# Optimization experiments

Hardware: AMD Instinct MI355X
Metric: run time of the kernel (lower is better)

Reference implementation:

```python
import jax, jax.numpy as jnp
import numpy as np

B, N, D, H, DH = 2, 2048, 1024, 16, 64
INNER = H * DH          # 1024
FF_INNER = 4 * D        # 4096 (GEGLU)
EPS = 1e-5


def setup_inputs() -> dict:
    key = jax.random.key(0)
    ks = jax.random.split(key, 12)
    s = D ** -0.5
    return {
        "x": jax.random.normal(ks[0], (B, N, D), jnp.float32),
        "Wq": jax.random.normal(ks[1], (D, INNER), jnp.float32) * s,
        "Wk": jax.random.normal(ks[2], (D, INNER), jnp.float32) * s,
        "Wv": jax.random.normal(ks[3], (D, INNER), jnp.float32) * s,
        "Wo": jax.random.normal(ks[4], (INNER, D), jnp.float32) * s,
        "bo": jnp.zeros((D,), jnp.float32),
        "ln1_g": jnp.ones((D,), jnp.float32),
        "ln1_b": jnp.zeros((D,), jnp.float32),
        "ln3_g": jnp.ones((D,), jnp.float32),
        "ln3_b": jnp.zeros((D,), jnp.float32),
        "Wff1": jax.random.normal(ks[5], (D, 2 * FF_INNER), jnp.float32) * s,
        "bff1": jnp.zeros((2 * FF_INNER,), jnp.float32),
        "Wff2": jax.random.normal(ks[6], (FF_INNER, D), jnp.float32) * (FF_INNER ** -0.5),
        "bff2": jnp.zeros((D,), jnp.float32),
    }


def _layernorm(x, g, b):
    mu = jnp.mean(x, axis=-1, keepdims=True)
    var = jnp.mean(jnp.square(x - mu), axis=-1, keepdims=True)
    return (x - mu) * jax.lax.rsqrt(var + EPS) * g + b


def reference(x, Wq, Wk, Wv, Wo, bo, ln1_g, ln1_b, ln3_g, ln3_b, Wff1, bff1, Wff2, bff2):
    scale = DH ** -0.5

    # norm1 + self-attention (attn1)
    x_features = _layernorm(x, ln1_g, ln1_b)
    q = (x_features @ Wq).reshape(B, N, H, DH)
    k = (x_features @ Wk).reshape(B, N, H, DH)
    v = (x_features @ Wv).reshape(B, N, H, DH)
    sim = jnp.einsum('bihd,bjhd->bhij', q, k) * scale      # (B,H,N,N) full scores
    attn = jax.nn.softmax(sim, axis=-1)
    inter_out = jnp.einsum('bhij,bjhd->bhid', attn, v)     # (B,H,N,DH)
    out = inter_out.transpose(0, 2, 1, 3).reshape(B, N, INNER)
    attended_x = out @ Wo + bo
    x = attended_x + x

    # norm3 + GEGLU feed-forward
    h = _layernorm(x, ln3_g, ln3_b) @ Wff1 + bff1
    a, gate = h[..., :FF_INNER], h[..., FF_INNER:]
    x = (a * jax.nn.gelu(gate, approximate=False)) @ Wff2 + bff2 + x

    # match torch return: q,k,v as (b h) n d, attn = inter_out (b h n d)
    q_bh = q.transpose(0, 2, 1, 3).reshape(B * H, N, DH)
    k_bh = k.transpose(0, 2, 1, 3).reshape(B * H, N, DH)
    v_bh = v.transpose(0, 2, 1, 3).reshape(B * H, N, DH)
    return (x, q_bh, k_bh, v_bh, inter_out, x_features)
```

## Files before the change

### kernel.cpp

```cpp
#include <hip/hip_runtime.h>
#include <hip/hip_bf16.h>

#define B_ 2
#define N_ 2048
#define D_ 1024
#define H_ 16
#define DH_ 64
#define M_ 4096
#define FFI_ 4096

typedef __attribute__((ext_vector_type(8))) short bh8;
typedef __attribute__((ext_vector_type(4))) float f4;

#define DEV static __device__ __forceinline__

DEV short f2bf(float f) { __hip_bfloat16 h = __float2bfloat16(f); return *reinterpret_cast<short*>(&h); }
DEV float bf2f(short s) { __hip_bfloat16 h = *reinterpret_cast<__hip_bfloat16*>(&s); return __bfloat162float(h); }

#define GLDS(gp, lp) __builtin_amdgcn_global_load_lds((const __attribute__((address_space(1))) void*)(gp), (__attribute__((address_space(3))) void*)(lp), 16, 0, 0)
#define MFMA16(a,b,c) __builtin_amdgcn_mfma_f32_16x16x32_bf16(a,b,c,0,0,0)

__global__ __launch_bounds__(256) void ln_kernel(const float* __restrict__ x,
    const float* __restrict__ g, const float* __restrict__ b,
    float* __restrict__ outF, short* __restrict__ outB)
{
  const int row = blockIdx.x;
  const int t = threadIdx.x;
  const float4 v = reinterpret_cast<const float4*>(x + (long)row*D_)[t];
  float s = v.x+v.y+v.z+v.w;
  float sq = v.x*v.x+v.y*v.y+v.z*v.z+v.w*v.w;
  #pragma unroll
  for (int o=32;o>0;o>>=1){ s += __shfl_xor(s,o); sq += __shfl_xor(sq,o); }
  __shared__ float red[8];
  const int w = t>>6, l = t&63;
  if (l==0){ red[w]=s; red[4+w]=sq; }
  __syncthreads();
  s  = red[0]+red[1]+red[2]+red[3];
  sq = red[4]+red[5]+red[6]+red[7];
  const float mu = s*(1.f/D_);
  const float rstd = rsqrtf(sq*(1.f/D_) - mu*mu + 1e-5f);
  const float4 gv = reinterpret_cast<const float4*>(g)[t];
  const float4 bv = reinterpret_cast<const float4*>(b)[t];
  float4 y;
  y.x=(v.x-mu)*rstd*gv.x+bv.x; y.y=(v.y-mu)*rstd*gv.y+bv.y;
  y.z=(v.z-mu)*rstd*gv.z+bv.z; y.w=(v.w-mu)*rstd*gv.w+bv.w;
  if (outF) reinterpret_cast<float4*>(outF + (long)row*D_)[t] = y;
  short4 ys; ys.x=f2bf(y.x); ys.y=f2bf(y.y); ys.z=f2bf(y.z); ys.w=f2bf(y.w);
  reinterpret_cast<short4*>(outB + (long)row*D_)[t] = ys;
}

__global__ __launch_bounds__(256) void transpose_cast(const float* __restrict__ in,
    short* __restrict__ out, int R, int C)
{
  __shared__ float tile[32][33];
  const int tx = threadIdx.x & 31, ty = threadIdx.x >> 5;
  const int c0 = blockIdx.x*32, r0 = blockIdx.y*32;
  #pragma unroll
  for (int i=0;i<4;i++) tile[ty+i*8][tx] = in[(long)(r0+ty+i*8)*C + c0+tx];
  __syncthreads();
  #pragma unroll
  for (int i=0;i<4;i++) out[(long)(c0+ty+i*8)*R + r0+tx] = f2bf(tile[tx][ty+i*8]);
}

DEV void gemm_core(const short* __restrict__ A, const short* __restrict__ BT, int K,
                   int m0, int n0, short* lA, short* lB, f4 (&acc)[4][4])
{
  const int t = threadIdx.x, w = t>>6, l = t&63;
  const int wrow = (w>>1)*64, wcol = (w&1)*64;
  const int lr = l&15, lk = (l>>4)*8;
  const int sr = t>>2, sc = (t&3)*8;
  const short* gA = A  + (long)(m0+sr)*K + sc;
  const short* gB = BT + (long)(n0+sr)*K + sc;
  #pragma unroll
  for (int i=0;i<4;i++)
    #pragma unroll
    for (int j=0;j<4;j++) acc[i][j] = f4{0.f,0.f,0.f,0.f};
  for (int k0=0; k0<K; k0+=32) {
    __syncthreads();
    GLDS(gA,              &lA[w*512]);
    GLDS(gA + (long)64*K, &lA[2048 + w*512]);
    GLDS(gB,              &lB[w*512]);
    GLDS(gB + (long)64*K, &lB[2048 + w*512]);
    gA += 32; gB += 32;
    asm volatile("s_waitcnt vmcnt(0)" ::: "memory");
    __syncthreads();
    bh8 af[4], bf_[4];
    #pragma unroll
    for (int i=0;i<4;i++) af[i]  = *reinterpret_cast<const bh8*>(&lA[(wrow+i*16+lr)*32 + lk]);
    #pragma unroll
    for (int j=0;j<4;j++) bf_[j] = *reinterpret_cast<const bh8*>(&lB[(wcol+j*16+lr)*32 + lk]);
    #pragma unroll
    for (int i=0;i<4;i++)
      #pragma unroll
      for (int j=0;j<4;j++)
        acc[i][j] = MFMA16(af[i], bf_[j], acc[i][j]);
  }
}

__global__ __launch_bounds__(256) void gemm_qkv(const short* __restrict__ A,
    const short* __restrict__ BTq, const short* __restrict__ BTk, const short* __restrict__ BTv,
    float* __restrict__ oQ, float* __restrict__ oK, float* __restrict__ oV,
    short* __restrict__ bQ, short* __restrict__ bK, short* __restrict__ bV)
{
  __shared__ short lA[4096], lB[4096];
  const int m0 = blockIdx.x*128;
  const int by = blockIdx.y, sel = by>>3, n0 = (by&7)*128;
  const short* BT = sel==0 ? BTq : (sel==1 ? BTk : BTv);
  float* oF = sel==0 ? oQ : (sel==1 ? oK : oV);
  short* oB = sel==0 ? bQ : (sel==1 ? bK : bV);
  const float bscale = sel==0 ? 0.125f : 1.0f;
  f4 acc[4][4];
  gemm_core(A, BT, 1024, m0, n0, lA, lB, acc);
  const int t = threadIdx.x, w = t>>6, l = t&63;
  const int wrow=(w>>1)*64, wcol=(w&1)*64, lr=l&15;
  #pragma unroll
  for (int i=0;i<4;i++)
    #pragma unroll
    for (int j=0;j<4;j++)
      #pragma unroll
      for (int r=0;r<4;r++) {
        const int grow = m0 + wrow + i*16 + (l>>4)*4 + r;
        const int gcol = n0 + wcol + j*16 + lr;
        const int bb = grow >> 11, nn = grow & 2047;
        const int hh = gcol >> 6, dd = gcol & 63;
        const long oi = ((long)(bb*H_ + hh)*N_ + nn)*DH_ + dd;
        const float v = acc[i][j][r];
        oF[oi] = v;
        oB[oi] = f2bf(v * bscale);
      }
}

template<int MODE>
__global__ __launch_bounds__(256) void gemm_bt(const short* __restrict__ A,
    const short* __restrict__ BT, int Ndim, int K,
    const float* __restrict__ bias, const float* __restrict__ resid,
    float* __restrict__ outF, short* __restrict__ outB)
{
  __shared__ short lA[4096], lB[4096];
  const int m0 = blockIdx.x*128, n0 = blockIdx.y*128;
  f4 acc[4][4];
  gemm_core(A, BT, K, m0, n0, lA, lB, acc);
  const int t = threadIdx.x, w=t>>6, l=t&63;
  const int wrow=(w>>1)*64, wcol=(w&1)*64, lr=l&15;
  #pragma unroll
  for (int i=0;i<4;i++)
    #pragma unroll
    for (int j=0;j<4;j++)
      #pragma unroll
      for (int r=0;r<4;r++) {
        const int grow = m0 + wrow + i*16 + (l>>4)*4 + r;
        const int gcol = n0 + wcol + j*16 + lr;
        const long oi = (long)grow*Ndim + gcol;
        const float v = acc[i][j][r] + bias[gcol];
        if (MODE==1) outF[oi] = v + resid[oi];
        else         outB[oi] = f2bf(v);
      }
}

__global__ __launch_bounds__(256) void attn_kernel(const short* __restrict__ Q,
    const short* __restrict__ Kb, const short* __restrict__ Vb,
    float* __restrict__ interOut, short* __restrict__ attnB)
{
  __shared__ short Kt[64*72];
  __shared__ short Vt[64*72];
  __shared__ short Pt[4*16*72];
  const int t = threadIdx.x, w = t>>6, l = t&63;
  const int bh = blockIdx.y;
  const int q0 = blockIdx.x*64;
  const int lr = l&15, lk = (l>>4)*8;
  const long base = (long)bh * (N_*DH_);
  const int qrow = q0 + w*16;
  bh8 qf0 = *reinterpret_cast<const bh8*>(&Q[base + (long)(qrow+lr)*DH_ + lk]);
  bh8 qf1 = *reinterpret_cast<const bh8*>(&Q[base + (long)(qrow+lr)*DH_ + 32 + lk]);
  f4 o[4];
  #pragma unroll
  for (int i=0;i<4;i++) o[i]=f4{0.f,0.f,0.f,0.f};
  float m_run[4], l_run[4];
  #pragma unroll
  for (int r=0;r<4;r++){ m_run[r]=-1e30f; l_run[r]=0.f; }
  const int srow = t>>3, sd = (t&7)*8;
  short* Pw = &Pt[w*16*72];
  for (int kt=0; kt<N_/64; kt++) {
    __syncthreads();
    #pragma unroll
    for (int it=0; it<2; it++) {
      const int j = it*32 + srow;
      const long grow = base + (long)(kt*64 + j)*DH_ + sd;
      int4 kv = *reinterpret_cast<const int4*>(&Kb[grow]);
      *reinterpret_cast<int4*>(&Kt[j*72 + sd]) = kv;
      int4 vv = *reinterpret_cast<const int4*>(&Vb[grow]);
      const short* vs = reinterpret_cast<const short*>(&vv);
      #pragma unroll
      for (int e=0;e<8;e++) Vt[(sd+e)*72 + j] = vs[e];
    }
    __syncthreads();
    f4 s[4];
    #pragma unroll
    for (int cb=0;cb<4;cb++) {
      bh8 kf0 = *reinterpret_cast<const bh8*>(&Kt[(cb*16+lr)*72 + lk]);
      bh8 kf1 = *reinterpret_cast<const bh8*>(&Kt[(cb*16+lr)*72 + 32 + lk]);
      f4 z = f4{0.f,0.f,0.f,0.f};
      z = MFMA16(qf0, kf0, z);
      z = MFMA16(qf1, kf1, z);
      s[cb] = z;
    }
    float mx[4];
    #pragma unroll
    for (int r=0;r<4;r++) mx[r] = fmaxf(fmaxf(s[0][r],s[1][r]), fmaxf(s[2][r],s[3][r]));
    #pragma unroll
    for (int mk=1; mk<16; mk<<=1)
      #pragma unroll
      for (int r=0;r<4;r++) mx[r] = fmaxf(mx[r], __shfl_xor(mx[r], mk));
    float rs[4];
    #pragma unroll
    for (int r=0;r<4;r++) {
      const float mn = fmaxf(m_run[r], mx[r]);
      const float al = __expf(m_run[r]-mn);
      m_run[r] = mn;
      l_run[r] *= al;
      float sum = 0.f;
      #pragma unroll
      for (int cb=0;cb<4;cb++) {
        const float pv = __expf(s[cb][r]-mn);
        sum += pv;
        Pw[((l>>4)*4 + r)*72 + cb*16 + lr] = f2bf(pv);
      }
      rs[r] = sum;
      #pragma unroll
      for (int cb=0;cb<4;cb++) o[cb][r] *= al;
    }
    #pragma unroll
    for (int mk=1; mk<16; mk<<=1)
      #pragma unroll
      for (int r=0;r<4;r++) rs[r] += __shfl_xor(rs[r], mk);
    #pragma unroll
    for (int r=0;r<4;r++) l_run[r] += rs[r];
    asm volatile("s_waitcnt lgkmcnt(0)" ::: "memory");
    __builtin_amdgcn_sched_barrier(0);
    bh8 pa0 = *reinterpret_cast<const bh8*>(&Pw[lr*72 + lk]);
    bh8 pa1 = *reinterpret_cast<const bh8*>(&Pw[lr*72 + 32 + lk]);
    #pragma unroll
    for (int db=0; db<4; db++) {
      bh8 vf0 = *reinterpret_cast<const bh8*>(&Vt[(db*16+lr)*72 + lk]);
      bh8 vf1 = *reinterpret_cast<const bh8*>(&Vt[(db*16+lr)*72 + 32 + lk]);
      o[db] = MFMA16(pa0, vf0, o[db]);
      o[db] = MFMA16(pa1, vf1, o[db]);
    }
  }
  const int bb = bh>>4, hh = bh&15;
  #pragma unroll
  for (int db=0; db<4; db++)
    #pragma unroll
    for (int r=0;r<4;r++) {
      const int n = qrow + (l>>4)*4 + r;
      const int d = db*16 + lr;
      const float v = o[db][r] / l_run[r];
      interOut[base + (long)n*DH_ + d] = v;
      attnB[((long)(bb*N_ + n))*D_*0 + ((long)(bb*N_ + n))*1024 + hh*DH_ + d] = f2bf(v);
    }
}

__global__ __launch_bounds__(256) void gelu_mul(const short* __restrict__ h, short* __restrict__ g)
{
  const long i = ((long)blockIdx.x*256 + threadIdx.x)*8;
  const long m = i >> 12;
  const int j = (int)(i & 4095);
  bh8 av = *reinterpret_cast<const bh8*>(&h[m*8192 + j]);
  bh8 gv = *reinterpret_cast<const bh8*>(&h[m*8192 + 4096 + j]);
  bh8 ov;
  #pragma unroll
  for (int e=0;e<8;e++) {
    const float a  = bf2f(av[e]);
    const float xg = bf2f(gv[e]);
    const float ge = 0.5f*xg*(1.f + erff(xg*0.70710678118f));
    ov[e] = f2bf(a*ge);
  }
  *reinterpret_cast<bh8*>(&g[i]) = ov;
}

extern "C" void kernel_launch(void* const* d_in, const int* in_sizes, int n_in,
                              void* d_out, int out_size, void* d_ws, size_t ws_size,
                              hipStream_t stream)
{
  const float* x    = (const float*)d_in[0];
  const float* Wq   = (const float*)d_in[1];
  const float* Wk   = (const float*)d_in[2];
  const float* Wv   = (const float*)d_in[3];
  const float* Wo   = (const float*)d_in[4];
  const float* bo   = (const float*)d_in[5];
  const float* ln1g = (const float*)d_in[6];
  const float* ln1b = (const float*)d_in[7];
  const float* ln3g = (const float*)d_in[8];
  const float* ln3b = (const float*)d_in[9];
  const float* Wff1 = (const float*)d_in[10];
  const float* bff1 = (const float*)d_in[11];
  const float* Wff2 = (const float*)d_in[12];
  const float* bff2 = (const float*)d_in[13];
  float* out = (float*)d_out;
  const long SZ = (long)M_*D_;
  float* out_x     = out;
  float* out_q     = out + SZ;
  float* out_k     = out + 2*SZ;
  float* out_v     = out + 3*SZ;
  float* out_inter = out + 4*SZ;
  float* out_xf    = out + 5*SZ;

  char* p = (char*)d_ws;
  auto alloc = [&](size_t bytes){ void* r = (void*)p; p += (bytes + 255) & ~(size_t)255; return r; };
  short* xf_bf  = (short*)alloc(SZ*2);
  short* q_bf   = (short*)alloc(SZ*2);
  short* k_bf   = (short*)alloc(SZ*2);
  short* v_bf   = (short*)alloc(SZ*2);
  short* at_bf  = (short*)alloc(SZ*2);
  float* x2     = (float*)alloc(SZ*4);
  short* x2n_bf = (short*)alloc(SZ*2);
  short* h_bf   = (short*)alloc((size_t)M_*8192*2);
  short* g_bf   = (short*)alloc((size_t)M_*4096*2);
  short* WqT    = (short*)alloc((size_t)1024*1024*2);
  short* WkT    = (short*)alloc((size_t)1024*1024*2);
  short* WvT    = (short*)alloc((size_t)1024*1024*2);
  short* WoT    = (short*)alloc((size_t)1024*1024*2);
  short* Wff1T  = (short*)alloc((size_t)8192*1024*2);
  short* Wff2T  = (short*)alloc((size_t)1024*4096*2);
  (void)in_sizes; (void)n_in; (void)out_size; (void)ws_size;

  dim3 blk(256);
  transpose_cast<<<dim3(32,32),  blk, 0, stream>>>(Wq,   WqT,   1024, 1024);
  transpose_cast<<<dim3(32,32),  blk, 0, stream>>>(Wk,   WkT,   1024, 1024);
  transpose_cast<<<dim3(32,32),  blk, 0, stream>>>(Wv,   WvT,   1024, 1024);
  transpose_cast<<<dim3(32,32),  blk, 0, stream>>>(Wo,   WoT,   1024, 1024);
  transpose_cast<<<dim3(256,32), blk, 0, stream>>>(Wff1, Wff1T, 1024, 8192);
  transpose_cast<<<dim3(32,128), blk, 0, stream>>>(Wff2, Wff2T, 4096, 1024);
  ln_kernel<<<M_, blk, 0, stream>>>(x, ln1g, ln1b, out_xf, xf_bf);
  gemm_qkv<<<dim3(32,24), blk, 0, stream>>>(xf_bf, WqT, WkT, WvT,
                                            out_q, out_k, out_v, q_bf, k_bf, v_bf);
  attn_kernel<<<dim3(32,32), blk, 0, stream>>>(q_bf, k_bf, v_bf, out_inter, at_bf);
  gemm_bt<1><<<dim3(32,8),  blk, 0, stream>>>(at_bf,  WoT,   1024, 1024, bo,   x,   x2,    nullptr);
  ln_kernel<<<M_, blk, 0, stream>>>(x2, ln3g, ln3b, nullptr, x2n_bf);
  gemm_bt<2><<<dim3(32,64), blk, 0, stream>>>(x2n_bf, Wff1T, 8192, 1024, bff1, nullptr, nullptr, h_bf);
  gelu_mul<<<8192, blk, 0, stream>>>(h_bf, g_bf);
  gemm_bt<1><<<dim3(32,8),  blk, 0, stream>>>(g_bf,   Wff2T, 1024, 4096, bff2, x2,  out_x, nullptr);
}
```

Measured before the change: 656.6 us.

## Swizzle attention K/V LDS tiles and load K via global_load_lds

Replaces the padded K and V shared-memory tiles with XOR-swizzled unpadded layouts. K is now loaded directly into LDS with global_load_lds, and V uses a swizzled transpose store. MFMA sections are wrapped in s_setprio raises. The goal is to cut LDS bank conflicts and register staging for K, at the cost of more complex index math and an explicit vmcnt wait.

```diff
diff --git a/kernel.cpp b/kernel.cpp
--- a/kernel.cpp
+++ b/kernel.cpp
@@ -161,13 +161,13 @@
     const short* __restrict__ Kb, const short* __restrict__ Vb,
     float* __restrict__ interOut, short* __restrict__ attnB)
 {
-  __shared__ short Kt[64*72];
-  __shared__ short Vt[64*72];
+  __shared__ short Kt[64*64];
+  __shared__ short Vt[64*64];
   __shared__ short Pt[4*16*72];
   const int t = threadIdx.x, w = t>>6, l = t&63;
   const int bh = blockIdx.y;
   const int q0 = blockIdx.x*64;
-  const int lr = l&15, lk = (l>>4)*8;
+  const int lr = l&15, lk = (l>>4)*8, g = l>>4;
   const long base = (long)bh * (N_*DH_);
   const int qrow = q0 + w*16;
   bh8 qf0 = *reinterpret_cast<const bh8*>(&Q[base + (long)(qrow+lr)*DH_ + lk]);
@@ -178,32 +178,48 @@
   float m_run[4], l_run[4];
   #pragma unroll
   for (int r=0;r<4;r++){ m_run[r]=-1e30f; l_run[r]=0.f; }
-  const int srow = t>>3, sd = (t&7)*8;
   short* Pw = &Pt[w*16*72];
+  const char* ldsK = (const char*)Kt;
+  const int beta0 = w*2048 + l*16;
+  const int srow = t>>3, sdp = t&7, sd = sdp*8;
   for (int kt=0; kt<N_/64; kt++) {
     __syncthreads();
+    {
+      const char* Kg = (const char*)(Kb + base + (long)kt*64*DH_);
+      #pragma unroll
+      for (int i=0;i<2;i++) {
+        const int beta = beta0 + i*1024;
+        const int krow = beta>>7, kpch = (beta>>4)&7;
+        GLDS(Kg + krow*128 + (kpch ^ (krow&7))*16, (char*)Kt + (w*2+i)*1024);
+      }
+    }
     #pragma unroll
     for (int it=0; it<2; it++) {
       const int j = it*32 + srow;
-      const long grow = base + (long)(kt*64 + j)*DH_ + sd;
-      int4 kv = *reinterpret_cast<const int4*>(&Kb[grow]);
-      *reinterpret_cast<int4*>(&Kt[j*72 + sd]) = kv;
-      int4 vv = *reinterpret_cast<const int4*>(&Vb[grow]);
+      const int4 vv = *reinterpret_cast<const int4*>(&Vb[base + (long)(kt*64+j)*DH_ + sd]);
       const short* vs = reinterpret_cast<const short*>(&vv);
-      #pragma unroll
-      for (int e=0;e<8;e++) Vt[(sd+e)*72 + j] = vs[e];
-    }
+      const int cb0 = (it*4 + (srow>>3)) ^ sdp;
+      const int jc  = srow & 7;
+      #pragma unroll
+      for (int e=0;e<8;e++)
+        Vt[(sd+e)*64 + ((cb0^e)<<3) + jc] = vs[e];
+    }
+    asm volatile("s_waitcnt vmcnt(0)" ::: "memory");
     __syncthreads();
     f4 s[4];
+    __builtin_amdgcn_s_setprio(1);
     #pragma unroll
     for (int cb=0;cb<4;cb++) {
-      bh8 kf0 = *reinterpret_cast<const bh8*>(&Kt[(cb*16+lr)*72 + lk]);
-      bh8 kf1 = *reinterpret_cast<const bh8*>(&Kt[(cb*16+lr)*72 + 32 + lk]);
+      const int krow = cb*16+lr;
+      const char* kr = ldsK + krow*128;
+      bh8 kf0 = *reinterpret_cast<const bh8*>(kr + ((g  )^(lr&7))*16);
+      bh8 kf1 = *reinterpret_cast<const bh8*>(kr + ((g+4)^(lr&7))*16);
       f4 z = f4{0.f,0.f,0.f,0.f};
       z = MFMA16(qf0, kf0, z);
       z = MFMA16(qf1, kf1, z);
       s[cb] = z;
     }
+    __builtin_amdgcn_s_setprio(0);
     float mx[4];
     #pragma unroll
     for (int r=0;r<4;r++) mx[r] = fmaxf(fmaxf(s[0][r],s[1][r]), fmaxf(s[2][r],s[3][r]));
@@ -240,11 +256,17 @@
     bh8 pa0 = *reinterpret_cast<const bh8*>(&Pw[lr*72 + lk]);
     bh8 pa1 = *reinterpret_cast<const bh8*>(&Pw[lr*72 + 32 + lk]);
     #pragma unroll
-    for (int db=0; db<4; db++) {
-      bh8 vf0 = *reinterpret_cast<const bh8*>(&Vt[(db*16+lr)*72 + lk]);
-      bh8 vf1 = *reinterpret_cast<const bh8*>(&Vt[(db*16+lr)*72 + 32 + lk]);
-      o[db] = MFMA16(pa0, vf0, o[db]);
-      o[db] = MFMA16(pa1, vf1, o[db]);
+    for (int kk=0; kk<2; kk++) {
+      const bh8 pa = kk ? pa1 : pa0;
+      __builtin_amdgcn_s_setprio(1);
+      #pragma unroll
+      for (int db=0; db<4; db++) {
+        const int dd = db*16 + lr;
+        const int ch = (kk*4 + g) ^ (dd&7) ^ ((dd>>3)&7);
+        bh8 vf = *reinterpret_cast<const bh8*>(&Vt[dd*64 + ch*8]);
+        o[db] = MFMA16(pa, vf, o[db]);
+      }
+      __builtin_amdgcn_s_setprio(0);
     }
   }
   const int bb = bh>>4, hh = bh&15;
@@ -256,7 +278,7 @@
       const int d = db*16 + lr;
       const float v = o[db][r] / l_run[r];
       interOut[base + (long)n*DH_ + d] = v;
-      attnB[((long)(bb*N_ + n))*D_*0 + ((long)(bb*N_ + n))*1024 + hh*DH_ + d] = f2bf(v);
+      attnB[(long)(bb*N_ + n)*1024 + hh*DH_ + d] = f2bf(v);
     }
 }
 
```

Measured after the change: 611.5 us. 1.07x faster.
